# Kernel optimization log

Measured on AMD Instinct MI355X. Metric: run time of the kernel, lower is better.

The kernel has to match this reference:

```python
import jax, jax.numpy as jnp
import numpy as np

N = 50000      # nodes
E = 800000     # edges (avg degree 16)
D = 128        # embed_dim
H = 8          # nhead
HD = D // H    # head dim = 16


def setup_inputs() -> dict:
    key = jax.random.key(0)
    ks = jax.random.split(key, 6)
    s = 1.0 / np.sqrt(D)  # ~xavier scale for square matrices
    return {
        "feats": jax.random.normal(ks[0], (N, D), jnp.float32),
        "edge_index": jax.random.randint(ks[1], (E, 2), 0, N, dtype=jnp.int64),
        "Wq": jax.random.normal(ks[2], (D, D), jnp.float32) * s,
        "bq": jnp.zeros((D,), jnp.float32),
        "Wk": jax.random.normal(ks[3], (D, D), jnp.float32) * s,
        "bk": jnp.zeros((D,), jnp.float32),
        "Wv": jax.random.normal(ks[4], (D, D), jnp.float32) * s,
        "bv": jnp.zeros((D,), jnp.float32),
        "Wo": jax.random.normal(ks[5], (D, D), jnp.float32) * s,
        "bo": jnp.zeros((D,), jnp.float32),
    }


def reference(feats, edge_index, Wq, bq, Wk, bk, Wv, bv, Wo, bo):
    # Projections (nn.Linear: x @ W.T + b), split into heads: [N, H, HD]
    q = (feats @ Wq.T + bq).reshape(N, H, HD)
    k = (feats @ Wk.T + bk).reshape(N, H, HD)
    v = (feats @ Wv.T + bv).reshape(N, H, HD)

    r = edge_index[:, 0]  # source nodes
    c = edge_index[:, 1]  # destination nodes (softmax / aggregation groups)

    # Per-edge, per-head dot-product scores: [E, H]
    scores = jnp.einsum('ehd,ehd->eh', q[c], k[r]) / np.sqrt(HD)

    # Custom scatter-softmax: src_max clamped to min 0; extra exp(-src_max) in denom
    smax = jnp.maximum(jax.ops.segment_max(scores, c, num_segments=N), 0.0)  # [N, H]
    ex = jnp.exp(scores - smax[c])                                           # [E, H]
    denom = jax.ops.segment_sum(ex, c, num_segments=N)                       # [N, H]
    attn = ex / (denom + jnp.exp(-smax))[c]                                  # [E, H]

    # Weighted V per edge, scatter-mean to destination nodes
    out_e = attn[:, :, None] * v[r]                      # [E, H, HD]
    agg = jax.ops.segment_sum(out_e, c, num_segments=N)  # [N, H, HD]
    cnt = jax.ops.segment_sum(jnp.ones((E,), jnp.float32), c, num_segments=N)
    agg = agg / jnp.maximum(cnt, 1.0)[:, None, None]

    return agg.reshape(N, D) @ Wo.T + bo
```

## Files before the change

kernel.cpp:

```cpp
#include <hip/hip_runtime.h>
#include <hip/hip_bf16.h>

#define N_NODES 50000
#define N_EDGES 800000
#define DIM 128
#define NHEAD 8
#define HDIM 16
#define ELL_PAD 64
#define ELL_SLICES 391
#define ELL_BLOCKS (8 * ELL_SLICES)
#define ROWTILES 3125
#define QKV_WAVES (ROWTILES * 3)
#define QKV_GRID ((QKV_WAVES + 3) / 4)

#define Q_OFF      0ull
#define KV_OFF     25600000ull
#define AGG_OFF    51200000ull
#define ELL_OFF    64000000ull
#define CNT_OFF    76800000ull
#define WBF_OFF    77000192ull
#define BIAS_OFF   77131264ull

typedef __attribute__((ext_vector_type(8))) short short8;
typedef __attribute__((ext_vector_type(4))) float floatx4;

__device__ inline float bflo2f(unsigned u) { return __uint_as_float(u << 16); }
__device__ inline float bfhi2f(unsigned u) { return __uint_as_float(u & 0xffff0000u); }
__device__ inline unsigned short f2bf(float f) {
    unsigned u = __float_as_uint(f);
    return (unsigned short)((u + 0x7fffu + ((u >> 16) & 1u)) >> 16);
}

__device__ inline void detect_flags(const void* feats, const void* edge,
                                    int& isbf, int& is32) {
    const unsigned short* f = (const unsigned short*)feats;
    const unsigned int* eg = (const unsigned int*)edge;
    int lane = threadIdx.x & 63;
    unsigned e = (f[lane] >> 7) & 0xFF;
    int junk = (e >= 0x90 || (e > 0 && e <= 0x60)) ? 1 : 0;
    unsigned long long jm = __ballot(junk);
    int nz = (lane < 32 && eg[2 * lane + 1] != 0) ? 1 : 0;
    unsigned long long nm = __ballot(nz);
    isbf = (jm == 0ull) ? 1 : 0;
    is32 = (nm != 0ull) ? 1 : 0;
}

__device__ inline void load_edge(const int* edge, int is32, int e, int& r, int& c) {
    if (is32) { int2 p = ((const int2*)edge)[e]; r = p.x; c = p.y; }
    else {
        const long long* p = (const long long*)edge;
        r = (int)p[2 * e]; c = (int)p[2 * e + 1];
    }
    if ((unsigned)r >= N_NODES) r = 0;
    if ((unsigned)c >= N_NODES) c = 0;
}

__device__ inline float ldf(const void* p, int isbf, int i) {
    return isbf ? __bfloat162float(((const __hip_bfloat16*)p)[i])
                : ((const float*)p)[i];
}

__device__ inline short8 ldfrag(const void* base, int isbf, size_t off) {
    if (isbf) return *(const short8*)((const unsigned short*)base + off);
    const float* f = (const float*)base + off;
    float4 f0 = *(const float4*)f;
    float4 f1 = *(const float4*)(f + 4);
    short8 a;
    a[0] = (short)f2bf(f0.x); a[1] = (short)f2bf(f0.y);
    a[2] = (short)f2bf(f0.z); a[3] = (short)f2bf(f0.w);
    a[4] = (short)f2bf(f1.x); a[5] = (short)f2bf(f1.y);
    a[6] = (short)f2bf(f1.z); a[7] = (short)f2bf(f1.w);
    return a;
}

__global__ __launch_bounds__(256) void ell_build(const void* feats, const int* edge,
                                                 const void* wq, const void* wk,
                                                 const void* wv, const void* wo,
                                                 const void* bq, const void* bk,
                                                 const void* bv, const void* bo,
                                                 int* cnt, int* ell,
                                                 unsigned short* wbf, float* bias) {
    int isbf, is32; detect_flags(feats, edge, isbf, is32);

    if (blockIdx.x >= ELL_BLOCKS) {
        int b2 = blockIdx.x - ELL_BLOCKS;
        if (b2 == 256) {
            for (int j = threadIdx.x; j < 512; j += 256) {
                int m2 = j >> 7;
                const void* bb = (m2 == 0) ? bq : (m2 == 1) ? bk : (m2 == 2) ? bv : bo;
                bias[j] = ldf(bb, isbf, j & 127);
            }
            return;
        }
        if (isbf) return;
        int idx = b2 * 256 + (int)threadIdx.x;
        int mm = idx >> 14, rem = idx & 16383;
        const void* wsrc = (mm == 0) ? wq : (mm == 1) ? wk : (mm == 2) ? wv : wo;
        wbf[idx] = f2bf(((const float*)wsrc)[rem]);
        return;
    }

    int pid = blockIdx.x & 7, slice = blockIdx.x >> 3;
    int base = slice * 2048 + (int)threadIdx.x;
    #pragma unroll
    for (int j = 0; j < 8; ++j) {
        int e = base + j * 256;
        if (e < N_EDGES) {
            int r, c; load_edge(edge, is32, e, r, c);
            if ((c & 7) == pid) {
                int slot = atomicAdd(cnt + c, 1);
                if (slot < ELL_PAD) ell[c * ELL_PAD + slot] = r;
            }
        }
    }
}

__global__ __launch_bounds__(256) void qkv_mfma(const void* feats_raw, const int* edge,
                                                const void* wq_raw, const void* wk_raw,
                                                const void* wv_raw,
                                                const unsigned short* wbf,
                                                const float* bias,
                                                float* q, unsigned short* kv_s) {
    int isbf, is32; detect_flags(feats_raw, edge, isbf, is32);
    int w = blockIdx.x * 4 + (threadIdx.x >> 6);
    if (w >= QKV_WAVES) return;
    int rowtile = w / 3;
    int m = w - rowtile * 3;
    int lane = threadIdx.x & 63;
    int mrow = lane & 15, quad = lane >> 4;
    int arow = rowtile * 16 + mrow;

    short8 a[4];
    #pragma unroll
    for (int kt = 0; kt < 4; ++kt)
        a[kt] = ldfrag(feats_raw, isbf, (size_t)arow * DIM + quad * 8 + kt * 32);

    const void* wraw = (m == 0) ? wq_raw : (m == 1) ? wk_raw : wv_raw;
    const unsigned short* wm = isbf ? (const unsigned short*)wraw : wbf + m * 16384;
    int soff = (m == 2) ? 16 : 0;

    for (int nt = 0; nt < 8; ++nt) {
        float b = bias[m * 128 + nt * 16 + mrow];
        floatx4 acc = {b, b, b, b};
        const unsigned short* wp = wm + (size_t)(nt * 16 + mrow) * DIM + quad * 8;
        #pragma unroll
        for (int kt = 0; kt < 4; ++kt) {
            short8 bf = *(const short8*)(wp + kt * 32);
            acc = __builtin_amdgcn_mfma_f32_16x16x32_bf16(a[kt], bf, acc, 0, 0, 0);
        }
        if (m == 0) {
            #pragma unroll
            for (int r4 = 0; r4 < 4; ++r4) {
                int row = rowtile * 16 + quad * 4 + r4;
                q[(size_t)row * DIM + nt * 16 + mrow] = acc[r4];
            }
        } else {
            #pragma unroll
            for (int r4 = 0; r4 < 4; ++r4) {
                int row = rowtile * 16 + quad * 4 + r4;
                kv_s[(size_t)row * 256 + nt * 32 + soff + mrow] = f2bf(acc[r4]);
            }
        }
    }
}

__global__ __launch_bounds__(256) void node_agg(const int* __restrict__ cnt,
                                                const int* __restrict__ ell,
                                                const float* __restrict__ q,
                                                const uint4* __restrict__ kvpack,
                                                uint4* __restrict__ agg_bf) {
    int node = (blockIdx.x * 256 + threadIdx.x) >> 6;
    int lane = threadIdx.x & 63;
    if (node >= N_NODES) return;
    int e = lane >> 3, h = lane & 7;

    float qv[16];
    const float4* qp = (const float4*)(q + (size_t)node * DIM + h * HDIM);
    #pragma unroll
    for (int i = 0; i < 4; ++i) {
        float4 tq = qp[i];
        qv[4 * i] = tq.x; qv[4 * i + 1] = tq.y; qv[4 * i + 2] = tq.z; qv[4 * i + 3] = tq.w;
    }

    int degt = cnt[node];
    int deg = degt < ELL_PAD ? degt : ELL_PAD;
    float l = 0.f;
    float acc[16];
    #pragma unroll
    for (int i = 0; i < 16; ++i) acc[i] = 0.f;

    const int* erow = ell + node * ELL_PAD;
    for (int i0 = 0; i0 < deg; i0 += 16) {
        int i1 = i0 + e, i2 = i0 + 8 + e;
        bool ok1 = i1 < deg, ok2 = i2 < deg;
        int r1 = ok1 ? erow[i1] : 0;
        int r2 = ok2 ? erow[i2] : 0;
        const uint4* kp1 = kvpack + (size_t)r1 * 32 + h * 4;
        const uint4* kp2 = kvpack + (size_t)r2 * 32 + h * 4;
        uint4 ka1 = kp1[0], kb1 = kp1[1], va1 = kp1[2], vb1 = kp1[3];
        uint4 ka2 = kp2[0], kb2 = kp2[1], va2 = kp2[2], vb2 = kp2[3];

        float s1 = 0.f;
        s1 += bflo2f(ka1.x) * qv[0]  + bfhi2f(ka1.x) * qv[1];
        s1 += bflo2f(ka1.y) * qv[2]  + bfhi2f(ka1.y) * qv[3];
        s1 += bflo2f(ka1.z) * qv[4]  + bfhi2f(ka1.z) * qv[5];
        s1 += bflo2f(ka1.w) * qv[6]  + bfhi2f(ka1.w) * qv[7];
        s1 += bflo2f(kb1.x) * qv[8]  + bfhi2f(kb1.x) * qv[9];
        s1 += bflo2f(kb1.y) * qv[10] + bfhi2f(kb1.y) * qv[11];
        s1 += bflo2f(kb1.z) * qv[12] + bfhi2f(kb1.z) * qv[13];
        s1 += bflo2f(kb1.w) * qv[14] + bfhi2f(kb1.w) * qv[15];
        float p1 = ok1 ? __expf(s1 * 0.25f) : 0.f;
        l += p1;
        acc[0]  += p1 * bflo2f(va1.x); acc[1]  += p1 * bfhi2f(va1.x);
        acc[2]  += p1 * bflo2f(va1.y); acc[3]  += p1 * bfhi2f(va1.y);
        acc[4]  += p1 * bflo2f(va1.z); acc[5]  += p1 * bfhi2f(va1.z);
        acc[6]  += p1 * bflo2f(va1.w); acc[7]  += p1 * bfhi2f(va1.w);
        acc[8]  += p1 * bflo2f(vb1.x); acc[9]  += p1 * bfhi2f(vb1.x);
        acc[10] += p1 * bflo2f(vb1.y); acc[11] += p1 * bfhi2f(vb1.y);
        acc[12] += p1 * bflo2f(vb1.z); acc[13] += p1 * bfhi2f(vb1.z);
        acc[14] += p1 * bflo2f(vb1.w); acc[15] += p1 * bfhi2f(vb1.w);

        float s2 = 0.f;
        s2 += bflo2f(ka2.x) * qv[0]  + bfhi2f(ka2.x) * qv[1];
        s2 += bflo2f(ka2.y) * qv[2]  + bfhi2f(ka2.y) * qv[3];
        s2 += bflo2f(ka2.z) * qv[4]  + bfhi2f(ka2.z) * qv[5];
        s2 += bflo2f(ka2.w) * qv[6]  + bfhi2f(ka2.w) * qv[7];
        s2 += bflo2f(kb2.x) * qv[8]  + bfhi2f(kb2.x) * qv[9];
        s2 += bflo2f(kb2.y) * qv[10] + bfhi2f(kb2.y) * qv[11];
        s2 += bflo2f(kb2.z) * qv[12] + bfhi2f(kb2.z) * qv[13];
        s2 += bflo2f(kb2.w) * qv[14] + bfhi2f(kb2.w) * qv[15];
        float p2 = ok2 ? __expf(s2 * 0.25f) : 0.f;
        l += p2;
        acc[0]  += p2 * bflo2f(va2.x); acc[1]  += p2 * bfhi2f(va2.x);
        acc[2]  += p2 * bflo2f(va2.y); acc[3]  += p2 * bfhi2f(va2.y);
        acc[4]  += p2 * bflo2f(va2.z); acc[5]  += p2 * bfhi2f(va2.z);
        acc[6]  += p2 * bflo2f(va2.w); acc[7]  += p2 * bfhi2f(va2.w);
        acc[8]  += p2 * bflo2f(vb2.x); acc[9]  += p2 * bfhi2f(vb2.x);
        acc[10] += p2 * bflo2f(vb2.y); acc[11] += p2 * bfhi2f(vb2.y);
        acc[12] += p2 * bflo2f(vb2.z); acc[13] += p2 * bfhi2f(vb2.z);
        acc[14] += p2 * bflo2f(vb2.w); acc[15] += p2 * bfhi2f(vb2.w);
    }

    #pragma unroll
    for (int m = 8; m < 64; m <<= 1) {
        l += __shfl_xor(l, m);
        #pragma unroll
        for (int i = 0; i < 16; ++i) acc[i] += __shfl_xor(acc[i], m);
    }

    float inv = 1.0f / ((1.0f + l) * (float)(degt > 0 ? degt : 1));
    if (e == 0) {
        unsigned o[8];
        #pragma unroll
        for (int i = 0; i < 8; ++i)
            o[i] = (unsigned)f2bf(acc[2 * i] * inv) | ((unsigned)f2bf(acc[2 * i + 1] * inv) << 16);
        uint4* op = agg_bf + (size_t)node * 16 + h * 2;
        op[0] = make_uint4(o[0], o[1], o[2], o[3]);
        op[1] = make_uint4(o[4], o[5], o[6], o[7]);
    }
}

__global__ __launch_bounds__(256) void out_mfma(const unsigned short* agg_bf,
                                                const void* feats, const int* edge,
                                                const void* wo_raw,
                                                const unsigned short* wbf,
                                                const float* bias, void* out) {
    int isbf, is32; detect_flags(feats, edge, isbf, is32);
    const unsigned short* W = isbf ? (const unsigned short*)wo_raw : wbf + 3 * 16384;
    int wave = threadIdx.x >> 6, lane = threadIdx.x & 63;
    int rbase = blockIdx.x * 64 + wave * 16;
    int mrow = lane & 15, quad = lane >> 4;
    int arow = rbase + mrow; if (arow >= N_NODES) arow = N_NODES - 1;

    short8 a[4];
    const unsigned short* ap = agg_bf + (size_t)arow * DIM + quad * 8;
    #pragma unroll
    for (int kt = 0; kt < 4; ++kt) a[kt] = *(const short8*)(ap + kt * 32);

    for (int nt = 0; nt < 8; ++nt) {
        float b = bias[3 * 128 + nt * 16 + mrow];
        floatx4 acc = {b, b, b, b};
        const unsigned short* wp = W + (size_t)(nt * 16 + mrow) * DIM + quad * 8;
        #pragma unroll
        for (int kt = 0; kt < 4; ++kt) {
            short8 bf = *(const short8*)(wp + kt * 32);
            acc = __builtin_amdgcn_mfma_f32_16x16x32_bf16(a[kt], bf, acc, 0, 0, 0);
        }
        if (isbf) {
            #pragma unroll
            for (int r4 = 0; r4 < 4; ++r4) {
                int row = rbase + quad * 4 + r4;
                if (row < N_NODES)
                    ((unsigned short*)out)[(size_t)row * DIM + nt * 16 + mrow] = f2bf(acc[r4]);
            }
        } else {
            #pragma unroll
            for (int r4 = 0; r4 < 4; ++r4) {
                int row = rbase + quad * 4 + r4;
                if (row < N_NODES) ((float*)out)[(size_t)row * DIM + nt * 16 + mrow] = acc[r4];
            }
        }
    }
}

extern "C" void kernel_launch(void* const* d_in, const int* in_sizes, int n_in,
                              void* d_out, int out_size, void* d_ws, size_t ws_size,
                              hipStream_t stream) {
    const void* feats = d_in[0];
    const int*  edge  = (const int*)d_in[1];
    const void* Wq = d_in[2]; const void* bq = d_in[3];
    const void* Wk = d_in[4]; const void* bk = d_in[5];
    const void* Wv = d_in[6]; const void* bv = d_in[7];
    const void* Wo = d_in[8]; const void* bo = d_in[9];

    char* ws = (char*)d_ws;
    float* q             = (float*)(ws + Q_OFF);
    unsigned short* kv_s = (unsigned short*)(ws + KV_OFF);
    unsigned short* aggb = (unsigned short*)(ws + AGG_OFF);
    int* ell             = (int*)(ws + ELL_OFF);
    int* cnt             = (int*)(ws + CNT_OFF);
    unsigned short* wbf  = (unsigned short*)(ws + WBF_OFF);
    float* bias          = (float*)(ws + BIAS_OFF);

    hipMemsetAsync(ws + CNT_OFF, 0, N_NODES * 4, stream);

    ell_build<<<ELL_BLOCKS + 257, 256, 0, stream>>>(feats, edge, Wq, Wk, Wv, Wo,
                                                    bq, bk, bv, bo, cnt, ell,
                                                    wbf, bias);

    qkv_mfma<<<QKV_GRID, 256, 0, stream>>>(feats, edge, Wq, Wk, Wv, wbf, bias,
                                           q, kv_s);

    node_agg<<<(N_NODES * 64 + 255) / 256, 256, 0, stream>>>(cnt, ell, q,
                                                             (const uint4*)(ws + KV_OFF),
                                                             (uint4*)aggb);

    out_mfma<<<(N_NODES + 63) / 64, 256, 0, stream>>>(aggb, feats, edge, Wo, wbf,
                                                      bias, d_out);
}
```

Before: 265.9 us.

## Fuse node aggregation with output projection and store Q in bf16

Merges the per-node attention aggregation and the output MFMA projection into one kernel. Each 1024-thread block handles 16 nodes, stages their aggregated rows in shared memory, then runs the Wo projection from that tile. This removes the global round trip of the aggregate buffer and one kernel launch. Q is now stored as bf16, which halves its write and read traffic but lowers score precision. The large blocks with a barrier may reduce occupancy and make waves idle while they wait for the slowest node in the block.

```diff
diff --git a/kernel.cpp b/kernel.cpp
--- a/kernel.cpp
+++ b/kernel.cpp
@@ -14,12 +14,11 @@
 #define QKV_GRID ((QKV_WAVES + 3) / 4)
 
 #define Q_OFF      0ull
-#define KV_OFF     25600000ull
-#define AGG_OFF    51200000ull
-#define ELL_OFF    64000000ull
-#define CNT_OFF    76800000ull
-#define WBF_OFF    77000192ull
-#define BIAS_OFF   77131264ull
+#define KV_OFF     12800000ull
+#define ELL_OFF    38400000ull
+#define CNT_OFF    51200000ull
+#define WBF_OFF    51400192ull
+#define BIAS_OFF   51531264ull
 
 typedef __attribute__((ext_vector_type(8))) short short8;
 typedef __attribute__((ext_vector_type(4))) float floatx4;
@@ -120,7 +119,7 @@
                                                 const void* wv_raw,
                                                 const unsigned short* wbf,
                                                 const float* bias,
-                                                float* q, unsigned short* kv_s) {
+                                                unsigned short* q_s, unsigned short* kv_s) {
     int isbf, is32; detect_flags(feats_raw, edge, isbf, is32);
     int w = blockIdx.x * 4 + (threadIdx.x >> 6);
     if (w >= QKV_WAVES) return;
@@ -152,7 +151,7 @@
             #pragma unroll
             for (int r4 = 0; r4 < 4; ++r4) {
                 int row = rowtile * 16 + quad * 4 + r4;
-                q[(size_t)row * DIM + nt * 16 + mrow] = acc[r4];
+                q_s[(size_t)row * DIM + nt * 16 + mrow] = f2bf(acc[r4]);
             }
         } else {
             #pragma unroll
@@ -164,23 +163,32 @@
     }
 }
 
-__global__ __launch_bounds__(256) void node_agg(const int* __restrict__ cnt,
-                                                const int* __restrict__ ell,
-                                                const float* __restrict__ q,
-                                                const uint4* __restrict__ kvpack,
-                                                uint4* __restrict__ agg_bf) {
-    int node = (blockIdx.x * 256 + threadIdx.x) >> 6;
-    int lane = threadIdx.x & 63;
-    if (node >= N_NODES) return;
+__global__ __launch_bounds__(1024) void node_agg_out(const int* __restrict__ cnt,
+                                                     const int* __restrict__ ell,
+                                                     const unsigned short* __restrict__ q_s,
+                                                     const uint4* __restrict__ kvpack,
+                                                     const void* feats, const int* edge,
+                                                     const void* wo_raw,
+                                                     const unsigned short* wbf,
+                                                     const float* bias, void* out) {
+    int isbf, is32; detect_flags(feats, edge, isbf, is32);
+    __shared__ unsigned short atile[16 * 136];
+
+    int wave = threadIdx.x >> 6, lane = threadIdx.x & 63;
+    int node = blockIdx.x * 16 + wave;
     int e = lane >> 3, h = lane & 7;
 
+    const uint4* qp = (const uint4*)(q_s + (size_t)node * DIM + h * HDIM);
+    uint4 q0 = qp[0], q1 = qp[1];
     float qv[16];
-    const float4* qp = (const float4*)(q + (size_t)node * DIM + h * HDIM);
-    #pragma unroll
-    for (int i = 0; i < 4; ++i) {
-        float4 tq = qp[i];
-        qv[4 * i] = tq.x; qv[4 * i + 1] = tq.y; qv[4 * i + 2] = tq.z; qv[4 * i + 3] = tq.w;
-    }
+    qv[0]  = bflo2f(q0.x); qv[1]  = bfhi2f(q0.x);
+    qv[2]  = bflo2f(q0.y); qv[3]  = bfhi2f(q0.y);
+    qv[4]  = bflo2f(q0.z); qv[5]  = bfhi2f(q0.z);
+    qv[6]  = bflo2f(q0.w); qv[7]  = bfhi2f(q0.w);
+    qv[8]  = bflo2f(q1.x); qv[9]  = bfhi2f(q1.x);
+    qv[10] = bflo2f(q1.y); qv[11] = bfhi2f(q1.y);
+    qv[12] = bflo2f(q1.z); qv[13] = bfhi2f(q1.z);
+    qv[14] = bflo2f(q1.w); qv[15] = bfhi2f(q1.w);
 
     int degt = cnt[node];
     int deg = degt < ELL_PAD ? degt : ELL_PAD;
@@ -254,51 +262,36 @@
         #pragma unroll
         for (int i = 0; i < 8; ++i)
             o[i] = (unsigned)f2bf(acc[2 * i] * inv) | ((unsigned)f2bf(acc[2 * i + 1] * inv) << 16);
-        uint4* op = agg_bf + (size_t)node * 16 + h * 2;
-        op[0] = make_uint4(o[0], o[1], o[2], o[3]);
-        op[1] = make_uint4(o[4], o[5], o[6], o[7]);
-    }
-}
-
-__global__ __launch_bounds__(256) void out_mfma(const unsigned short* agg_bf,
-                                                const void* feats, const int* edge,
-                                                const void* wo_raw,
-                                                const unsigned short* wbf,
-                                                const float* bias, void* out) {
-    int isbf, is32; detect_flags(feats, edge, isbf, is32);
-    const unsigned short* W = isbf ? (const unsigned short*)wo_raw : wbf + 3 * 16384;
-    int wave = threadIdx.x >> 6, lane = threadIdx.x & 63;
-    int rbase = blockIdx.x * 64 + wave * 16;
-    int mrow = lane & 15, quad = lane >> 4;
-    int arow = rbase + mrow; if (arow >= N_NODES) arow = N_NODES - 1;
-
-    short8 a[4];
-    const unsigned short* ap = agg_bf + (size_t)arow * DIM + quad * 8;
-    #pragma unroll
-    for (int kt = 0; kt < 4; ++kt) a[kt] = *(const short8*)(ap + kt * 32);
-
-    for (int nt = 0; nt < 8; ++nt) {
+        uint4* dst = (uint4*)(atile + wave * 136 + h * 16);
+        dst[0] = make_uint4(o[0], o[1], o[2], o[3]);
+        dst[1] = make_uint4(o[4], o[5], o[6], o[7]);
+    }
+    __syncthreads();
+
+    if (wave < 8) {
+        int nt = wave;
+        int mrow = lane & 15, quad = lane >> 4;
+        short8 a[4];
+        const unsigned short* ap = atile + mrow * 136 + quad * 8;
+        #pragma unroll
+        for (int kt = 0; kt < 4; ++kt) a[kt] = *(const short8*)(ap + kt * 32);
+
+        const unsigned short* W = isbf ? (const unsigned short*)wo_raw : wbf + 3 * 16384;
         float b = bias[3 * 128 + nt * 16 + mrow];
-        floatx4 acc = {b, b, b, b};
+        floatx4 oacc = {b, b, b, b};
         const unsigned short* wp = W + (size_t)(nt * 16 + mrow) * DIM + quad * 8;
         #pragma unroll
         for (int kt = 0; kt < 4; ++kt) {
             short8 bf = *(const short8*)(wp + kt * 32);
-            acc = __builtin_amdgcn_mfma_f32_16x16x32_bf16(a[kt], bf, acc, 0, 0, 0);
-        }
-        if (isbf) {
-            #pragma unroll
-            for (int r4 = 0; r4 < 4; ++r4) {
-                int row = rbase + quad * 4 + r4;
-                if (row < N_NODES)
-                    ((unsigned short*)out)[(size_t)row * DIM + nt * 16 + mrow] = f2bf(acc[r4]);
-            }
-        } else {
-            #pragma unroll
-            for (int r4 = 0; r4 < 4; ++r4) {
-                int row = rbase + quad * 4 + r4;
-                if (row < N_NODES) ((float*)out)[(size_t)row * DIM + nt * 16 + mrow] = acc[r4];
-            }
+            oacc = __builtin_amdgcn_mfma_f32_16x16x32_bf16(a[kt], bf, oacc, 0, 0, 0);
+        }
+        #pragma unroll
+        for (int r4 = 0; r4 < 4; ++r4) {
+            int row = blockIdx.x * 16 + quad * 4 + r4;
+            if (isbf)
+                ((unsigned short*)out)[(size_t)row * DIM + nt * 16 + mrow] = f2bf(oacc[r4]);
+            else
+                ((float*)out)[(size_t)row * DIM + nt * 16 + mrow] = oacc[r4];
         }
     }
 }
@@ -314,9 +307,8 @@
     const void* Wo = d_in[8]; const void* bo = d_in[9];
 
     char* ws = (char*)d_ws;
-    float* q             = (float*)(ws + Q_OFF);
+    unsigned short* q_s  = (unsigned short*)(ws + Q_OFF);
     unsigned short* kv_s = (unsigned short*)(ws + KV_OFF);
-    unsigned short* aggb = (unsigned short*)(ws + AGG_OFF);
     int* ell             = (int*)(ws + ELL_OFF);
     int* cnt             = (int*)(ws + CNT_OFF);
     unsigned short* wbf  = (unsigned short*)(ws + WBF_OFF);
@@ -329,12 +321,9 @@
                                                     wbf, bias);
 
     qkv_mfma<<<QKV_GRID, 256, 0, stream>>>(feats, edge, Wq, Wk, Wv, wbf, bias,
-                                           q, kv_s);
-
-    node_agg<<<(N_NODES * 64 + 255) / 256, 256, 0, stream>>>(cnt, ell, q,
-                                                             (const uint4*)(ws + KV_OFF),
-                                                             (uint4*)aggb);
-
-    out_mfma<<<(N_NODES + 63) / 64, 256, 0, stream>>>(aggb, feats, edge, Wo, wbf,
-                                                      bias, d_out);
-}
+                                           q_s, kv_s);
+
+    node_agg_out<<<ROWTILES, 1024, 0, stream>>>(cnt, ell, q_s,
+                                                (const uint4*)(ws + KV_OFF),
+                                                feats, edge, Wo, wbf, bias, d_out);
+}
```

Measured after the change: 281.5 us. +5.9%, slower.
